# Kernel tuning notes

Measured on AMD Instinct MI355X. Metric: run time of the kernel, lower is better.

The kernel has to match this reference:

```python
import jax, jax.numpy as jnp
import numpy as np

B = 16; IMG = 127; INC = 64; GROUP = 1; STRIDE = 2; PAD = 1; KS = 3
G = INC // GROUP            # number of ScannCore blocks
S = KS * KS                 # patch_size (attention dim) = 9
SPN = (IMG + 2 * PAD - KS) // STRIDE + 1   # 64
PN = SPN * SPN              # patch_num = 4096
L = GROUP * PN              # sequence length per core


def setup_inputs() -> dict:
    key = jax.random.key(0)
    ks = jax.random.split(key, 9)
    sc = 1.0 / np.sqrt(S)
    x = jax.random.normal(ks[0], (B, INC, IMG, IMG), jnp.float32)
    Wq = jax.random.uniform(ks[1], (G, S, S), jnp.float32, -sc, sc)
    bq = jax.random.uniform(ks[2], (G, S), jnp.float32, -sc, sc)
    Wk = jax.random.uniform(ks[3], (G, S, S), jnp.float32, -sc, sc)
    bk = jax.random.uniform(ks[4], (G, S), jnp.float32, -sc, sc)
    Wv = jax.random.uniform(ks[5], (G, S, S), jnp.float32, -sc, sc)
    bv = jax.random.uniform(ks[6], (G, S), jnp.float32, -sc, sc)
    Wo = jax.random.uniform(ks[7], (G, S, 1), jnp.float32, -sc, sc)
    bo = jax.random.uniform(ks[8], (G, 1), jnp.float32, -sc, sc)
    return dict(x=x, Wq=Wq, bq=bq, Wk=Wk, bk=bk, Wv=Wv, bv=bv, Wo=Wo, bo=bo)


def reference(x, Wq, bq, Wk, bk, Wv, bv, Wo, bo):
    # F.unfold equivalent: [B, INC*S, SPN, SPN] with feature dim ordered (C, kh, kw)
    patches = jax.lax.conv_general_dilated_patches(
        x, (KS, KS), (STRIDE, STRIDE), [(PAD, PAD), (PAD, PAD)])
    t = patches.reshape(B, INC, S, PN)
    # split channels into G groups of GROUP, move patch axis before patch-pixel axis
    t = t.reshape(B, G, GROUP, S, PN).transpose(0, 1, 2, 4, 3).reshape(B, G, L, S)
    # batched tiny single-head attention across all G cores at once
    Q = jnp.einsum('bgls,gst->bglt', t, Wq) + bq[None, :, None, :]
    Km = jnp.einsum('bgls,gst->bglt', t, Wk) + bk[None, :, None, :]
    V = jnp.einsum('bgls,gst->bglt', t, Wv) + bv[None, :, None, :]
    # energy = K^T @ Q over the L axis -> [B, G, S, S]
    energy = jnp.einsum('bgls,bglt->bgst', Km, Q)
    attn = jax.nn.softmax(energy, axis=-1)   # dropout is identity in eval
    # (attn @ V^T)^T -> [B, G, L, S]
    a = jnp.einsum('bgst,bglt->bgls', attn, V)
    out = jnp.einsum('bgls,gso->bglo', a, Wo) + bo[None, :, None, :]  # [B,G,L,1]
    # faithful reshape/permute of original: [B, spn, spn, group] -> [B, group, spn, spn]
    out = out.reshape(B, G, SPN, SPN, GROUP).transpose(0, 1, 4, 2, 3)
    return out.reshape(B, INC, SPN, SPN)
```

## Files before the change

kernel.cpp:

```cpp
#include <hip/hip_runtime.h>
#include <math.h>

#define NB       16
#define IMG      127
#define INC      64
#define PN       4096
#define NTHREADS 512
#define PPT      8

#define GLOBAL_AS __attribute__((address_space(1)))
#define LDS_AS    __attribute__((address_space(3)))

__device__ __forceinline__ constexpr int symidx(int p, int q) {
    return p * 9 - (p * (p - 1)) / 2 + (q - p);
}

__device__ __forceinline__ float wave_reduce_sum(float v) {
#define DPP_ADD(ctrl)                                                          \
    v += __builtin_bit_cast(float, __builtin_amdgcn_update_dpp(                \
             0, __builtin_bit_cast(int, v), (ctrl), 0xf, 0xf, true))
    DPP_ADD(0x111);
    DPP_ADD(0x112);
    DPP_ADD(0x114);
    DPP_ADD(0x118);
    DPP_ADD(0x142);
    DPP_ADD(0x143);
#undef DPP_ADD
    return v;
}

__global__ void __launch_bounds__(NTHREADS, 4)
scann_fused(const float* __restrict__ x,
            const float* __restrict__ Wq, const float* __restrict__ bq,
            const float* __restrict__ Wk, const float* __restrict__ bk,
            const float* __restrict__ Wv, const float* __restrict__ bv,
            const float* __restrict__ Wo, const float* __restrict__ bo,
            float* __restrict__ out)
{
    __shared__ float plane[IMG * IMG];
    __shared__ float red[8 * 54];
    __shared__ float Msh[45];
    __shared__ float msh[9];
    __shared__ float Wq_s[81], Wk_s[81], Wv_s[81];
    __shared__ float bq_s[9], bk_s[9], bv_s[9], Wo_s[9];
    __shared__ float en[81];
    __shared__ float at[81];
    __shared__ float wt[9];
    __shared__ float u_s[9];
    __shared__ float c_s;

    const int bg  = blockIdx.x;
    const int g   = bg & 63;
    const int tid = threadIdx.x;
    const int ow  = tid & 63;
    const int wv  = tid >> 6;
    const int oh0 = wv * PPT;

    const float* __restrict__ xp = x + (size_t)bg * (IMG * IMG);

    #pragma unroll
    for (int j = 0; j < 31; ++j) {
        __builtin_amdgcn_global_load_lds(
            (const GLOBAL_AS void*)(xp + j * NTHREADS + tid),
            (LDS_AS void*)(&plane[j * NTHREADS + wv * 64]), 4, 0, 0);
    }
    if (tid < IMG * IMG - 31 * NTHREADS)
        plane[31 * NTHREADS + tid] = xp[31 * NTHREADS + tid];

    if (tid < 81) {
        Wq_s[tid] = Wq[g * 81 + tid];
        Wk_s[tid] = Wk[g * 81 + tid];
        Wv_s[tid] = Wv[g * 81 + tid];
    } else if (tid >= 128 && tid < 137) {
        const int i = tid - 128;
        bq_s[i] = bq[g * 9 + i];
        bk_s[i] = bk[g * 9 + i];
        bv_s[i] = bv[g * 9 + i];
        Wo_s[i] = Wo[g * 9 + i];
    }
    __syncthreads();

    const int  iw0 = ow * 2 - 1;
    const bool c0  = (ow > 0), c2 = (ow < 63);

    float Macc[45], macc[9];
    #pragma unroll
    for (int i = 0; i < 45; ++i) Macc[i] = 0.f;
    #pragma unroll
    for (int i = 0; i < 9; ++i)  macc[i] = 0.f;

    {
        float v[9];
        #pragma unroll
        for (int kh = 0; kh < 3; ++kh) {
            const int  ih  = oh0 * 2 - 1 + kh;
            const bool rok = (unsigned)ih < (unsigned)IMG;
            v[kh * 3 + 0] = (rok && c0) ? plane[ih * IMG + iw0]     : 0.f;
            v[kh * 3 + 1] =  rok        ? plane[ih * IMG + iw0 + 1] : 0.f;
            v[kh * 3 + 2] = (rok && c2) ? plane[ih * IMG + iw0 + 2] : 0.f;
        }
        #pragma unroll
        for (int k = 0; k < PPT; ++k) {
            int idx = 0;
            #pragma unroll
            for (int p = 0; p < 9; ++p) {
                macc[p] += v[p];
                #pragma unroll
                for (int q = p; q < 9; ++q)
                    Macc[idx++] += v[p] * v[q];
            }
            if (k < PPT - 1) {
                v[0] = v[6]; v[1] = v[7]; v[2] = v[8];
                #pragma unroll
                for (int kh = 1; kh < 3; ++kh) {
                    const int  ih  = (oh0 + k + 1) * 2 - 1 + kh;
                    const bool rok = (unsigned)ih < (unsigned)IMG;
                    v[kh * 3 + 0] = (rok && c0) ? plane[ih * IMG + iw0]     : 0.f;
                    v[kh * 3 + 1] =  rok        ? plane[ih * IMG + iw0 + 1] : 0.f;
                    v[kh * 3 + 2] = (rok && c2) ? plane[ih * IMG + iw0 + 2] : 0.f;
                }
            }
        }
    }

    #pragma unroll
    for (int i = 0; i < 45; ++i) Macc[i] = wave_reduce_sum(Macc[i]);
    #pragma unroll
    for (int i = 0; i < 9; ++i)  macc[i] = wave_reduce_sum(macc[i]);
    if (ow == 63) {
        #pragma unroll
        for (int i = 0; i < 45; ++i) red[wv * 54 + i]      = Macc[i];
        #pragma unroll
        for (int i = 0; i < 9; ++i)  red[wv * 54 + 45 + i] = macc[i];
    }
    __syncthreads();
    if (tid < 54) {
        float s = 0.f;
        #pragma unroll
        for (int w = 0; w < 8; ++w) s += red[w * 54 + tid];
        if (tid < 45) Msh[tid]      = s;
        else          msh[tid - 45] = s;
    }
    __syncthreads();

    if (tid < 81) {
        const int s = tid / 9, t = tid % 9;
        float km = 0.f, qm = 0.f;
        #pragma unroll
        for (int p = 0; p < 9; ++p) km += Wk_s[p * 9 + s] * msh[p];
        #pragma unroll
        for (int q = 0; q < 9; ++q) qm += Wq_s[q * 9 + t] * msh[q];
        float e = (float)PN * bk_s[s] * bq_s[t] + km * bq_s[t] + bk_s[s] * qm;
        #pragma unroll
        for (int p = 0; p < 9; ++p) {
            float acc = 0.f;
            #pragma unroll
            for (int q = 0; q < 9; ++q) {
                const int a_ = p < q ? p : q, b_ = p < q ? q : p;
                acc += Msh[symidx(a_, b_)] * Wq_s[q * 9 + t];
            }
            e += Wk_s[p * 9 + s] * acc;
        }
        en[tid] = e;
    }
    __syncthreads();

    if (tid < 9) {
        const int s = tid;
        float mx = en[s * 9];
        #pragma unroll
        for (int t = 1; t < 9; ++t) mx = fmaxf(mx, en[s * 9 + t]);
        float ex[9], sum = 0.f;
        #pragma unroll
        for (int t = 0; t < 9; ++t) { ex[t] = expf(en[s * 9 + t] - mx); sum += ex[t]; }
        const float inv = 1.f / sum;
        #pragma unroll
        for (int t = 0; t < 9; ++t) at[s * 9 + t] = ex[t] * inv;
    }
    __syncthreads();

    if (tid < 9) {
        const int t = tid;
        float w = 0.f;
        #pragma unroll
        for (int s = 0; s < 9; ++s) w += at[s * 9 + t] * Wo_s[s];
        wt[t] = w;
    }
    __syncthreads();

    if (tid < 9) {
        const int p = tid;
        float uu = 0.f;
        #pragma unroll
        for (int t = 0; t < 9; ++t) uu += Wv_s[p * 9 + t] * wt[t];
        u_s[p] = uu;
    }
    if (tid == 63) {
        float cc = bo[g];
        #pragma unroll
        for (int t = 0; t < 9; ++t) cc += bv_s[t] * wt[t];
        c_s = cc;
    }
    __syncthreads();

    float ur[9];
    #pragma unroll
    for (int i = 0; i < 9; ++i) ur[i] = u_s[i];
    const float cc = c_s;
    float* __restrict__ op = out + (size_t)bg * PN;

    {
        float v[9];
        #pragma unroll
        for (int kh = 0; kh < 3; ++kh) {
            const int  ih  = oh0 * 2 - 1 + kh;
            const bool rok = (unsigned)ih < (unsigned)IMG;
            v[kh * 3 + 0] = (rok && c0) ? plane[ih * IMG + iw0]     : 0.f;
            v[kh * 3 + 1] =  rok        ? plane[ih * IMG + iw0 + 1] : 0.f;
            v[kh * 3 + 2] = (rok && c2) ? plane[ih * IMG + iw0 + 2] : 0.f;
        }
        #pragma unroll
        for (int k = 0; k < PPT; ++k) {
            float o = cc;
            #pragma unroll
            for (int i = 0; i < 9; ++i) o += v[i] * ur[i];
            op[(oh0 + k) * 64 + ow] = o;
            if (k < PPT - 1) {
                v[0] = v[6]; v[1] = v[7]; v[2] = v[8];
                #pragma unroll
                for (int kh = 1; kh < 3; ++kh) {
                    const int  ih  = (oh0 + k + 1) * 2 - 1 + kh;
                    const bool rok = (unsigned)ih < (unsigned)IMG;
                    v[kh * 3 + 0] = (rok && c0) ? plane[ih * IMG + iw0]     : 0.f;
                    v[kh * 3 + 1] =  rok        ? plane[ih * IMG + iw0 + 1] : 0.f;
                    v[kh * 3 + 2] = (rok && c2) ? plane[ih * IMG + iw0 + 2] : 0.f;
                }
            }
        }
    }
}

extern "C" void kernel_launch(void* const* d_in, const int* in_sizes, int n_in,
                              void* d_out, int out_size, void* d_ws, size_t ws_size,
                              hipStream_t stream) {
    (void)in_sizes; (void)n_in; (void)d_ws; (void)ws_size; (void)out_size;
    const float* x  = (const float*)d_in[0];
    const float* Wq = (const float*)d_in[1];
    const float* bq = (const float*)d_in[2];
    const float* Wk = (const float*)d_in[3];
    const float* bk = (const float*)d_in[4];
    const float* Wv = (const float*)d_in[5];
    const float* bv = (const float*)d_in[6];
    const float* Wo = (const float*)d_in[7];
    const float* bo = (const float*)d_in[8];
    float* out = (float*)d_out;

    dim3 grid(NB * INC), block(NTHREADS);
    hipLaunchKernelGGL(scann_fused, grid, block, 0, stream,
                       x, Wq, bq, Wk, bk, Wv, bv, Wo, bo, out);
}
```

Baseline: 39.65 us.

## Split Gram accumulation into two passes, widen LDS loads, single-wave attention tail

The 45-entry Gram accumulation is split into two passes over the plane (rows 0-2 and rows 3-8), which lowers the peak number of live accumulator registers at the cost of reading LDS twice. The global-to-LDS plane copy now uses 16-byte global_load_lds transfers after a small alignment prologue, with a scalar tail loop for the remainder. The post-reduction attention math (M·Wq product, energy, softmax, output weights) runs inside wave 0 with an MW intermediate, replacing several block-wide barriers with intra-wave sequencing. Together these aim to cut register pressure, load instruction count and synchronization overhead.

```diff
diff --git a/kernel.cpp b/kernel.cpp
--- a/kernel.cpp
+++ b/kernel.cpp
@@ -3,6 +3,7 @@
 
 #define NB       16
 #define IMG      127
+#define PLANE    (IMG * IMG)
 #define INC      64
 #define PN       4096
 #define NTHREADS 512
@@ -29,6 +30,16 @@
     return v;
 }
 
+#define LOAD_ROW(d0, d1, d2, ihv)                                              \
+    {                                                                          \
+        const int  ih_ = (ihv);                                                \
+        const bool rok = (unsigned)ih_ < (unsigned)IMG;                        \
+        const int  ba  = ih_ * IMG + iw0;                                      \
+        d0 = (rok && c0) ? plane[ba]     : 0.f;                                \
+        d1 =  rok        ? plane[ba + 1] : 0.f;                                \
+        d2 = (rok && c2) ? plane[ba + 2] : 0.f;                                \
+    }
+
 __global__ void __launch_bounds__(NTHREADS, 4)
 scann_fused(const float* __restrict__ x,
             const float* __restrict__ Wq, const float* __restrict__ bq,
@@ -37,17 +48,15 @@
             const float* __restrict__ Wo, const float* __restrict__ bo,
             float* __restrict__ out)
 {
-    __shared__ float plane[IMG * IMG];
+    __shared__ float plane[PLANE];
     __shared__ float red[8 * 54];
     __shared__ float Msh[45];
     __shared__ float msh[9];
+    __shared__ float MW[81];
     __shared__ float Wq_s[81], Wk_s[81], Wv_s[81];
     __shared__ float bq_s[9], bk_s[9], bv_s[9], Wo_s[9];
-    __shared__ float en[81];
-    __shared__ float at[81];
-    __shared__ float wt[9];
-    __shared__ float u_s[9];
-    __shared__ float c_s;
+    __shared__ float en[81], at[81], wt[9], u_s[9];
+    __shared__ float c_s, bo_sh;
 
     const int bg  = blockIdx.x;
     const int g   = bg & 63;
@@ -56,16 +65,22 @@
     const int wv  = tid >> 6;
     const int oh0 = wv * PPT;
 
-    const float* __restrict__ xp = x + (size_t)bg * (IMG * IMG);
-
+    const float* __restrict__ xp = x + (size_t)bg * PLANE;
+
+    const int a0 = (4 - (bg & 3)) & 3;
+    if (tid < a0) plane[tid] = xp[tid];
     #pragma unroll
-    for (int j = 0; j < 31; ++j) {
+    for (int j = 0; j < 7; ++j) {
         __builtin_amdgcn_global_load_lds(
-            (const GLOBAL_AS void*)(xp + j * NTHREADS + tid),
-            (LDS_AS void*)(&plane[j * NTHREADS + wv * 64]), 4, 0, 0);
-    }
-    if (tid < IMG * IMG - 31 * NTHREADS)
-        plane[31 * NTHREADS + tid] = xp[31 * NTHREADS + tid];
+            (const GLOBAL_AS void*)(xp + a0 + (j * NTHREADS + tid) * 4),
+            (LDS_AS void*)(&plane[a0 + (j * NTHREADS + wv * 64) * 4]), 16, 0, 0);
+    }
+    {
+        const int base = a0 + 7 * NTHREADS * 4;
+        const int cnt  = PLANE - base;
+        for (int i = tid; i < cnt; i += NTHREADS)
+            plane[base + i] = xp[base + i];
+    }
 
     if (tid < 81) {
         Wq_s[tid] = Wq[g * 81 + tid];
@@ -77,129 +92,152 @@
         bk_s[i] = bk[g * 9 + i];
         bv_s[i] = bv[g * 9 + i];
         Wo_s[i] = Wo[g * 9 + i];
+    } else if (tid == 192) {
+        bo_sh = bo[g];
     }
     __syncthreads();
 
     const int  iw0 = ow * 2 - 1;
     const bool c0  = (ow > 0), c2 = (ow < 63);
-
-    float Macc[45], macc[9];
-    #pragma unroll
-    for (int i = 0; i < 45; ++i) Macc[i] = 0.f;
-    #pragma unroll
-    for (int i = 0; i < 9; ++i)  macc[i] = 0.f;
-
-    {
-        float v[9];
-        #pragma unroll
-        for (int kh = 0; kh < 3; ++kh) {
-            const int  ih  = oh0 * 2 - 1 + kh;
-            const bool rok = (unsigned)ih < (unsigned)IMG;
-            v[kh * 3 + 0] = (rok && c0) ? plane[ih * IMG + iw0]     : 0.f;
-            v[kh * 3 + 1] =  rok        ? plane[ih * IMG + iw0 + 1] : 0.f;
-            v[kh * 3 + 2] = (rok && c2) ? plane[ih * IMG + iw0 + 2] : 0.f;
-        }
+    const int  ih0 = oh0 * 2 - 1;
+
+    {
+        float mA[24], mm[9], v[9];
+        #pragma unroll
+        for (int i = 0; i < 24; ++i) mA[i] = 0.f;
+        #pragma unroll
+        for (int i = 0; i < 9; ++i)  mm[i] = 0.f;
+        LOAD_ROW(v[0], v[1], v[2], ih0 + 0);
+        LOAD_ROW(v[3], v[4], v[5], ih0 + 1);
+        LOAD_ROW(v[6], v[7], v[8], ih0 + 2);
+        #pragma unroll
+        for (int k = 0; k < PPT; ++k) {
+            #pragma unroll
+            for (int p = 0; p < 9; ++p) mm[p] += v[p];
+            int idx = 0;
+            #pragma unroll
+            for (int p = 0; p < 3; ++p)
+                #pragma unroll
+                for (int q = p; q < 9; ++q)
+                    mA[idx++] += v[p] * v[q];
+            if (k < PPT - 1) {
+                v[0] = v[6]; v[1] = v[7]; v[2] = v[8];
+                LOAD_ROW(v[3], v[4], v[5], ih0 + 2 * (k + 1) + 1);
+                LOAD_ROW(v[6], v[7], v[8], ih0 + 2 * (k + 1) + 2);
+            }
+        }
+        #pragma unroll
+        for (int i = 0; i < 24; ++i) mA[i] = wave_reduce_sum(mA[i]);
+        #pragma unroll
+        for (int i = 0; i < 9; ++i)  mm[i] = wave_reduce_sum(mm[i]);
+        if (ow == 63) {
+            #pragma unroll
+            for (int i = 0; i < 24; ++i) red[wv * 54 + i]      = mA[i];
+            #pragma unroll
+            for (int i = 0; i < 9; ++i)  red[wv * 54 + 45 + i] = mm[i];
+        }
+    }
+
+    {
+        float mB[21], v[9];
+        #pragma unroll
+        for (int i = 0; i < 21; ++i) mB[i] = 0.f;
+        LOAD_ROW(v[0], v[1], v[2], ih0 + 0);
+        LOAD_ROW(v[3], v[4], v[5], ih0 + 1);
+        LOAD_ROW(v[6], v[7], v[8], ih0 + 2);
         #pragma unroll
         for (int k = 0; k < PPT; ++k) {
             int idx = 0;
             #pragma unroll
-            for (int p = 0; p < 9; ++p) {
-                macc[p] += v[p];
+            for (int p = 3; p < 9; ++p)
                 #pragma unroll
                 for (int q = p; q < 9; ++q)
-                    Macc[idx++] += v[p] * v[q];
-            }
+                    mB[idx++] += v[p] * v[q];
             if (k < PPT - 1) {
                 v[0] = v[6]; v[1] = v[7]; v[2] = v[8];
-                #pragma unroll
-                for (int kh = 1; kh < 3; ++kh) {
-                    const int  ih  = (oh0 + k + 1) * 2 - 1 + kh;
-                    const bool rok = (unsigned)ih < (unsigned)IMG;
-                    v[kh * 3 + 0] = (rok && c0) ? plane[ih * IMG + iw0]     : 0.f;
-                    v[kh * 3 + 1] =  rok        ? plane[ih * IMG + iw0 + 1] : 0.f;
-                    v[kh * 3 + 2] = (rok && c2) ? plane[ih * IMG + iw0 + 2] : 0.f;
+                LOAD_ROW(v[3], v[4], v[5], ih0 + 2 * (k + 1) + 1);
+                LOAD_ROW(v[6], v[7], v[8], ih0 + 2 * (k + 1) + 2);
+            }
+        }
+        #pragma unroll
+        for (int i = 0; i < 21; ++i) mB[i] = wave_reduce_sum(mB[i]);
+        if (ow == 63) {
+            #pragma unroll
+            for (int i = 0; i < 21; ++i) red[wv * 54 + 24 + i] = mB[i];
+        }
+    }
+    __syncthreads();
+
+    if (wv == 0) {
+        const int lane = ow;
+        if (lane < 54) {
+            float s = 0.f;
+            #pragma unroll
+            for (int w = 0; w < 8; ++w) s += red[w * 54 + lane];
+            if (lane < 45) Msh[lane]      = s;
+            else           msh[lane - 45] = s;
+        }
+        #pragma unroll
+        for (int r = 0; r < 2; ++r) {
+            const int e = lane + r * 64;
+            if (e < 81) {
+                const int p = e / 9, t = e % 9;
+                float acc = 0.f;
+                #pragma unroll
+                for (int q = 0; q < 9; ++q) {
+                    const int a_ = p < q ? p : q, b_ = p < q ? q : p;
+                    acc += Msh[symidx(a_, b_)] * Wq_s[q * 9 + t];
                 }
-            }
-        }
-    }
-
-    #pragma unroll
-    for (int i = 0; i < 45; ++i) Macc[i] = wave_reduce_sum(Macc[i]);
-    #pragma unroll
-    for (int i = 0; i < 9; ++i)  macc[i] = wave_reduce_sum(macc[i]);
-    if (ow == 63) {
-        #pragma unroll
-        for (int i = 0; i < 45; ++i) red[wv * 54 + i]      = Macc[i];
-        #pragma unroll
-        for (int i = 0; i < 9; ++i)  red[wv * 54 + 45 + i] = macc[i];
-    }
-    __syncthreads();
-    if (tid < 54) {
-        float s = 0.f;
-        #pragma unroll
-        for (int w = 0; w < 8; ++w) s += red[w * 54 + tid];
-        if (tid < 45) Msh[tid]      = s;
-        else          msh[tid - 45] = s;
-    }
-    __syncthreads();
-
-    if (tid < 81) {
-        const int s = tid / 9, t = tid % 9;
-        float km = 0.f, qm = 0.f;
-        #pragma unroll
-        for (int p = 0; p < 9; ++p) km += Wk_s[p * 9 + s] * msh[p];
-        #pragma unroll
-        for (int q = 0; q < 9; ++q) qm += Wq_s[q * 9 + t] * msh[q];
-        float e = (float)PN * bk_s[s] * bq_s[t] + km * bq_s[t] + bk_s[s] * qm;
-        #pragma unroll
-        for (int p = 0; p < 9; ++p) {
-            float acc = 0.f;
-            #pragma unroll
-            for (int q = 0; q < 9; ++q) {
-                const int a_ = p < q ? p : q, b_ = p < q ? q : p;
-                acc += Msh[symidx(a_, b_)] * Wq_s[q * 9 + t];
-            }
-            e += Wk_s[p * 9 + s] * acc;
-        }
-        en[tid] = e;
-    }
-    __syncthreads();
-
-    if (tid < 9) {
-        const int s = tid;
-        float mx = en[s * 9];
-        #pragma unroll
-        for (int t = 1; t < 9; ++t) mx = fmaxf(mx, en[s * 9 + t]);
-        float ex[9], sum = 0.f;
-        #pragma unroll
-        for (int t = 0; t < 9; ++t) { ex[t] = expf(en[s * 9 + t] - mx); sum += ex[t]; }
-        const float inv = 1.f / sum;
-        #pragma unroll
-        for (int t = 0; t < 9; ++t) at[s * 9 + t] = ex[t] * inv;
-    }
-    __syncthreads();
-
-    if (tid < 9) {
-        const int t = tid;
-        float w = 0.f;
-        #pragma unroll
-        for (int s = 0; s < 9; ++s) w += at[s * 9 + t] * Wo_s[s];
-        wt[t] = w;
-    }
-    __syncthreads();
-
-    if (tid < 9) {
-        const int p = tid;
-        float uu = 0.f;
-        #pragma unroll
-        for (int t = 0; t < 9; ++t) uu += Wv_s[p * 9 + t] * wt[t];
-        u_s[p] = uu;
-    }
-    if (tid == 63) {
-        float cc = bo[g];
-        #pragma unroll
-        for (int t = 0; t < 9; ++t) cc += bv_s[t] * wt[t];
-        c_s = cc;
+                MW[e] = acc;
+            }
+        }
+        #pragma unroll
+        for (int r = 0; r < 2; ++r) {
+            const int e = lane + r * 64;
+            if (e < 81) {
+                const int s = e / 9, t = e % 9;
+                float km = 0.f, qm = 0.f, acc = 0.f;
+                #pragma unroll
+                for (int p = 0; p < 9; ++p) {
+                    km  += Wk_s[p * 9 + s] * msh[p];
+                    qm  += Wq_s[p * 9 + t] * msh[p];
+                    acc += Wk_s[p * 9 + s] * MW[p * 9 + t];
+                }
+                en[e] = acc + (float)PN * bk_s[s] * bq_s[t] + km * bq_s[t] + bk_s[s] * qm;
+            }
+        }
+        if (lane < 9) {
+            const int s = lane;
+            float mx = en[s * 9];
+            #pragma unroll
+            for (int t = 1; t < 9; ++t) mx = fmaxf(mx, en[s * 9 + t]);
+            float ex[9], sum = 0.f;
+            #pragma unroll
+            for (int t = 0; t < 9; ++t) { ex[t] = expf(en[s * 9 + t] - mx); sum += ex[t]; }
+            const float inv = 1.f / sum;
+            #pragma unroll
+            for (int t = 0; t < 9; ++t) at[s * 9 + t] = ex[t] * inv;
+        }
+        if (lane < 9) {
+            const int t = lane;
+            float w = 0.f;
+            #pragma unroll
+            for (int s = 0; s < 9; ++s) w += at[s * 9 + t] * Wo_s[s];
+            wt[t] = w;
+        }
+        if (lane < 9) {
+            const int p = lane;
+            float uu = 0.f;
+            #pragma unroll
+            for (int t = 0; t < 9; ++t) uu += Wv_s[p * 9 + t] * wt[t];
+            u_s[p] = uu;
+        }
+        if (lane == 12) {
+            float cc = bo_sh;
+            #pragma unroll
+            for (int t = 0; t < 9; ++t) cc += bv_s[t] * wt[t];
+            c_s = cc;
+        }
     }
     __syncthreads();
 
@@ -211,14 +249,9 @@
 
     {
         float v[9];
-        #pragma unroll
-        for (int kh = 0; kh < 3; ++kh) {
-            const int  ih  = oh0 * 2 - 1 + kh;
-            const bool rok = (unsigned)ih < (unsigned)IMG;
-            v[kh * 3 + 0] = (rok && c0) ? plane[ih * IMG + iw0]     : 0.f;
-            v[kh * 3 + 1] =  rok        ? plane[ih * IMG + iw0 + 1] : 0.f;
-            v[kh * 3 + 2] = (rok && c2) ? plane[ih * IMG + iw0 + 2] : 0.f;
-        }
+        LOAD_ROW(v[0], v[1], v[2], ih0 + 0);
+        LOAD_ROW(v[3], v[4], v[5], ih0 + 1);
+        LOAD_ROW(v[6], v[7], v[8], ih0 + 2);
         #pragma unroll
         for (int k = 0; k < PPT; ++k) {
             float o = cc;
@@ -227,14 +260,8 @@
             op[(oh0 + k) * 64 + ow] = o;
             if (k < PPT - 1) {
                 v[0] = v[6]; v[1] = v[7]; v[2] = v[8];
-                #pragma unroll
-                for (int kh = 1; kh < 3; ++kh) {
-                    const int  ih  = (oh0 + k + 1) * 2 - 1 + kh;
-                    const bool rok = (unsigned)ih < (unsigned)IMG;
-                    v[kh * 3 + 0] = (rok && c0) ? plane[ih * IMG + iw0]     : 0.f;
-                    v[kh * 3 + 1] =  rok        ? plane[ih * IMG + iw0 + 1] : 0.f;
-                    v[kh * 3 + 2] = (rok && c2) ? plane[ih * IMG + iw0 + 2] : 0.f;
-                }
+                LOAD_ROW(v[3], v[4], v[5], ih0 + 2 * (k + 1) + 1);
+                LOAD_ROW(v[6], v[7], v[8], ih0 + 2 * (k + 1) + 2);
             }
         }
     }
```

Result: slower. 41.09 us (+3.6%).
